# Optimization experiments

Measured on AMD Instinct MI355X. Metric: run time of the kernel, lower is better.

## Reference

```python
import jax, jax.numpy as jnp
import numpy as np

T, B, Y, X, C = 3, 2, 192, 192, 128
H, F = 8, 16
HF = H * F
RY = RX = 2
PH, PW = 2 * RY + 1, 2 * RX + 1
S = PH * PW  # 25 spatial offsets per frame


def setup_inputs() -> dict:
    key = jax.random.key(0)
    ks = jax.random.split(key, 7)
    sc_w = 1.0 / np.sqrt(C)
    return {
        "frames": jax.random.normal(ks[0], (T, B, Y, X, C), jnp.float32),
        "Wq": jax.random.normal(ks[1], (C, HF), jnp.float32) * sc_w,
        "Wk": jax.random.normal(ks[2], (C, HF), jnp.float32) * sc_w,
        "Wv": jax.random.normal(ks[3], (C, HF), jnp.float32) * sc_w,
        "Wout": jax.random.normal(ks[4], (HF, C), jnp.float32) * (1.0 / np.sqrt(HF)),
        "temp_emb": jax.random.normal(ks[5], (T, HF), jnp.float32) * 0.02,
        "spatial_emb": jax.random.normal(ks[6], (S, HF), jnp.float32) * 0.02,
    }


def _attention(frames, Wq, Wk, Wv, Wout, temp_emb, spatial_emb):
    dtype = frames.dtype
    scale = jnp.asarray(1.0 / np.sqrt(F), dtype)
    # 1x1 convs == channel-wise dense
    Kf = jnp.einsum('tbyxc,cd->tbyxd', frames, Wk).reshape(T, B, Y, X, H, F)
    Vf = jnp.einsum('tbyxc,cd->tbyxd', frames, Wv).reshape(T, B, Y, X, H, F)
    Qf = jnp.einsum('tbyxc,cd->tbyxd', frames, Wq).reshape(T, B, Y, X, H, F)
    # temporal embedding: added to K per frame, and to Q per query frame (queries = all frames)
    t_emb = temp_emb.reshape(T, 1, 1, 1, H, F)
    Kf = Kf + t_emb
    # query spatial embedding: relative position of query inside its clipped patch
    yc = jnp.clip(jnp.arange(Y), RY, Y - RY - 1)  # patch center rows [Y]
    xc = jnp.clip(jnp.arange(X), RX, X - RX - 1)  # patch center cols [X]
    y_rel = jnp.arange(Y) - yc + RY
    x_rel = jnp.arange(X) - xc + RX
    q_sidx = y_rel[:, None] * PW + x_rel[None, :]  # [Y,X] in [0,S)
    q_s = spatial_emb[q_sidx].reshape(1, 1, Y, X, H, F)
    Qf = Qf + q_s + t_emb
    # spatial offsets, row-major (dy outer, dx inner) so offset index s matches spatial_emb row
    offs = np.array([[dy, dx] for dy in range(-RY, RY + 1) for dx in range(-RX, RX + 1)], np.int32)
    y_gather = yc[None, :] + jnp.asarray(offs[:, 0])[:, None]  # [S,Y], always in-bounds
    x_gather = xc[None, :] + jnp.asarray(offs[:, 1])[:, None]  # [S,X]
    k_s_emb = spatial_emb.reshape(S, H, F)

    def step(carry, s_in):
        m, l, acc = carry
        yg, xg, ks = s_in  # yg:[Y] xg:[X] ks:[H,F]
        Kg = Kf[:, :, yg][:, :, :, xg] + ks       # [T,B,Y,X,H,F]
        Vg = Vf[:, :, yg][:, :, :, xg]            # [T,B,Y,X,H,F]
        sc = jnp.einsum('qbyxhf,tbyxhf->qtbyxh', Qf, Kg) * scale  # [nQ,T,B,Y,X,H]
        m_new = jnp.maximum(m, sc.max(axis=1))    # [nQ,B,Y,X,H]
        p = jnp.exp(sc - m_new[:, None])
        alpha = jnp.exp(m - m_new)
        l = l * alpha + p.sum(axis=1)
        acc = acc * alpha[..., None] + jnp.einsum('qtbyxh,tbyxhf->qbyxhf', p, Vg)
        return (m_new, l, acc), None

    m0 = jnp.full((T, B, Y, X, H), -1e9, dtype)
    l0 = jnp.zeros((T, B, Y, X, H), dtype)
    acc0 = jnp.zeros((T, B, Y, X, H, F), dtype)
    (m, l, acc), _ = jax.lax.scan(step, (m0, l0, acc0), (y_gather, x_gather, k_s_emb))
    out = (acc / l[..., None]).reshape(T, B, Y, X, HF)
    return jnp.einsum('tbyxd,dc->tbyxc', out, Wout)  # [nQ=T,B,Y,X,C]


def reference(frames, Wq, Wk, Wv, Wout, temp_emb, spatial_emb):
    return _attention(frames, Wq, Wk, Wv, Wout, temp_emb, spatial_emb)
```

## Files before the change

### kernel.cpp

```cpp
#include <hip/hip_runtime.h>
#include <cstdint>
#include <cstddef>

#define T_ 3
#define B_ 2
#define Y_ 192
#define X_ 192
#define YX_ 36864
#define N_ 221184
#define NS_ 73728

typedef __attribute__((ext_vector_type(8))) short short8;
typedef __attribute__((ext_vector_type(4))) float f32x4;
typedef __attribute__((ext_vector_type(2))) float f32x2;
typedef unsigned short u16;
typedef unsigned int u32;

__device__ __forceinline__ u16 f2bf(float f){
  u32 x = __builtin_bit_cast(u32, f);
  x += 0x7fffu + ((x >> 16) & 1u);
  return (u16)(x >> 16);
}
__device__ __forceinline__ float bflo(u32 u){ return __builtin_bit_cast(float, u << 16); }
__device__ __forceinline__ float bfhi(u32 u){ return __builtin_bit_cast(float, u & 0xffff0000u); }
__device__ __forceinline__ f32x2 bfp(u32 u){
  f32x2 r; r.x = bflo(u); r.y = bfhi(u); return r;
}
__device__ __forceinline__ int clampi(int v, int lo, int hi){ return v < lo ? lo : (v > hi ? hi : v); }
__device__ __forceinline__ f32x2 shfl2(f32x2 v, int m){
  f32x2 r; r.x = __shfl_xor(v.x, m); r.y = __shfl_xor(v.y, m); return r;
}

#if __has_builtin(__builtin_amdgcn_fdot2_f32_bf16)
typedef __attribute__((ext_vector_type(2))) __bf16 bf16x2;
__device__ __forceinline__ float dot2bf(u32 a, u32 b, float c){
  return __builtin_amdgcn_fdot2_f32_bf16(__builtin_bit_cast(bf16x2, a),
                                         __builtin_bit_cast(bf16x2, b), c, false);
}
#else
__device__ __forceinline__ float dot2bf(u32 a, u32 b, float c){
  return fmaf(bfhi(a), bfhi(b), fmaf(bflo(a), bflo(b), c));
}
#endif

#if __has_builtin(__builtin_amdgcn_exp2f)
__device__ __forceinline__ float fexp2(float x){ return __builtin_amdgcn_exp2f(x); }
#else
__device__ __forceinline__ float fexp2(float x){ return exp2f(x); }
#endif

#define QSCALE 0.36067376022224085f

__global__ __launch_bounds__(256) void wt_kernel(
    const float* __restrict__ Wq, const float* __restrict__ Wk,
    const float* __restrict__ Wv, const float* __restrict__ Wo,
    const float* __restrict__ spatial_emb, u16* __restrict__ WT, u16* __restrict__ se_bf){
  int idx = blockIdx.x * 256 + threadIdx.x;
  if (idx < 65536){
    int g = idx >> 14;
    int r = (idx >> 7) & 127;
    int c = idx & 127;
    const float* W = (g == 0) ? Wq : (g == 1) ? Wk : (g == 2) ? Wv : Wo;
    WT[g * 16384 + c * 128 + r] = f2bf(W[r * 128 + c]);
  } else if (idx < 65536 + 3200){
    se_bf[idx - 65536] = f2bf(spatial_emb[idx - 65536]);
  }
}

__global__ __launch_bounds__(256, 2) void qkv_kernel(
    const float* __restrict__ frames, const u16* __restrict__ WT,
    u16* __restrict__ Qb, u16* __restrict__ Kb, u16* __restrict__ Vb,
    const float* __restrict__ temp_emb, const float* __restrict__ spatial_emb){
  __shared__ float tile[128 * 128];
  const int tid = threadIdx.x;
  const int w = tid >> 6, l = tid & 63;
  const int l16 = l & 15, lg = l >> 4;
  const int m0 = blockIdx.x * 128;

  short8 af[4][2];
  #pragma unroll
  for (int ks = 0; ks < 4; ++ks)
    #pragma unroll
    for (int mr = 0; mr < 2; ++mr){
      const float* ap = frames + (size_t)(m0 + w * 32 + mr * 16 + l16) * 128 + ks * 32 + lg * 8;
      const f32x4 a0 = *(const f32x4*)ap;
      const f32x4 a1 = *(const f32x4*)(ap + 4);
      short8 t;
      t[0] = (short)f2bf(a0[0]); t[1] = (short)f2bf(a0[1]);
      t[2] = (short)f2bf(a0[2]); t[3] = (short)f2bf(a0[3]);
      t[4] = (short)f2bf(a1[0]); t[5] = (short)f2bf(a1[1]);
      t[6] = (short)f2bf(a1[2]); t[7] = (short)f2bf(a1[3]);
      af[ks][mr] = t;
    }

  #pragma unroll
  for (int g = 0; g < 3; ++g){
    const u16* wt = WT + g * 16384;
    f32x4 acc[2][8];
    #pragma unroll
    for (int mr = 0; mr < 2; ++mr)
      #pragma unroll
      for (int nf = 0; nf < 8; ++nf)
        acc[mr][nf] = (f32x4){0.f, 0.f, 0.f, 0.f};

    #pragma unroll
    for (int ks = 0; ks < 4; ++ks)
      #pragma unroll
      for (int nf = 0; nf < 8; ++nf){
        const short8 bf = *(const short8*)(wt + (nf * 16 + l16) * 128 + ks * 32 + lg * 8);
        acc[0][nf] = __builtin_amdgcn_mfma_f32_16x16x32_bf16(af[ks][0], bf, acc[0][nf], 0, 0, 0);
        acc[1][nf] = __builtin_amdgcn_mfma_f32_16x16x32_bf16(af[ks][1], bf, acc[1][nf], 0, 0, 0);
      }

    if (g > 0) __syncthreads();
    #pragma unroll
    for (int mr = 0; mr < 2; ++mr)
      #pragma unroll
      for (int nf = 0; nf < 8; ++nf)
        #pragma unroll
        for (int i = 0; i < 4; ++i)
          tile[(w * 32 + mr * 16 + lg * 4 + i) * 128 + nf * 16 + l16] = acc[mr][nf][i];
    __syncthreads();

    u16* outp = (g == 0) ? Qb : (g == 1) ? Kb : Vb;
    #pragma unroll
    for (int it = 0; it < 16; ++it){
      const int idx = it * 256 + tid;
      const int r = idx >> 5;
      const int c4 = (idx & 31) * 4;
      f32x4 v = *(const f32x4*)&tile[r * 128 + c4];
      const int p = m0 + r;
      const int t = p / (B_ * YX_);
      if (g <= 1){
        const float* te = temp_emb + t * 128 + c4;
        v[0] += te[0]; v[1] += te[1]; v[2] += te[2]; v[3] += te[3];
      }
      if (g == 0){
        const int yx = p % YX_;
        const int y = yx / X_, x = yx % X_;
        const int yrel = y - clampi(y, 2, Y_ - 3) + 2;
        const int xrel = x - clampi(x, 2, X_ - 3) + 2;
        const float* se = spatial_emb + (yrel * 5 + xrel) * 128 + c4;
        v[0] = (v[0] + se[0]) * QSCALE; v[1] = (v[1] + se[1]) * QSCALE;
        v[2] = (v[2] + se[2]) * QSCALE; v[3] = (v[3] + se[3]) * QSCALE;
      }
      uint2 pk;
      pk.x = (u32)f2bf(v[0]) | ((u32)f2bf(v[1]) << 16);
      pk.y = (u32)f2bf(v[2]) | ((u32)f2bf(v[3]) << 16);
      *(uint2*)(outp + (size_t)p * 128 + c4) = pk;
    }
  }
}

__global__ __attribute__((amdgpu_waves_per_eu(4, 4))) __launch_bounds__(256) void attn_kernel(
    const u16* __restrict__ Kb, const u16* __restrict__ Vb,
    u16* __restrict__ Qb, const u16* __restrict__ se_bf){
  __shared__ float qse[4][2][600];
  __shared__ u32 tbl[80];
  const int tid = threadIdx.x;
  const int w = tid >> 6, l = tid & 63;
  const int s2 = l >> 5, slot = (l >> 3) & 3, h = l & 7;

  if (tid < 80){
    const int kk = tid > 74 ? 74 : tid;
    const int t = kk / 25, s = kk - t * 25;
    const int dy = s / 5, dx = s - dy * 5;
    tbl[tid] = (u32)((((t * (B_ * Y_) + dy) * X_ + dx) * 256) | (s * 8));
  }

  const int site = blockIdx.x * 8 + w * 2 + s2;
  const int b = site / YX_;
  const int yx = site % YX_;
  const int y = yx / X_, x = yx % X_;
  const int yc = clampi(y, 2, 189), xc = clampi(x, 2, 189);
  const u32 sbase = (u32)(((b * Y_ + (yc - 2)) * X_ + (xc - 2)) * 256 + h * 32);
  const char* Kc = (const char*)Kb;
  const char* Vc = (const char*)Vb;

  u32 qp[3][8];
  #pragma unroll
  for (int q = 0; q < 3; ++q){
    const u16* qptr = Qb + ((size_t)((q * B_ + b) * Y_ + y) * X_ + x) * 128 + h * 16;
    const uint4 a = *(const uint4*)qptr;
    const uint4 c = *(const uint4*)(qptr + 8);
    qp[q][0] = a.x; qp[q][1] = a.y; qp[q][2] = a.z; qp[q][3] = a.w;
    qp[q][4] = c.x; qp[q][5] = c.y; qp[q][6] = c.z; qp[q][7] = c.w;
  }

  float* qsl = &qse[w][s2][0];
  #pragma unroll
  for (int sj = 0; sj < 7; ++sj){
    const int so = sj * 4 + slot;
    if (so < 25){
      const u16* sp = se_bf + so * 128 + h * 16;
      const uint4 e0 = *(const uint4*)sp;
      const uint4 e1 = *(const uint4*)(sp + 8);
      u32 ep[8] = {e0.x, e0.y, e0.z, e0.w, e1.x, e1.y, e1.z, e1.w};
      #pragma unroll
      for (int q = 0; q < 3; ++q){
        float d = 0.f;
        #pragma unroll
        for (int i = 0; i < 8; ++i) d = dot2bf(qp[q][i], ep[i], d);
        qsl[q * 200 + so * 8 + h] = d;
      }
    }
  }
  __syncthreads();

  float ll[3] = {0.f, 0.f, 0.f};
  f32x2 acc[3][8];
  #pragma unroll
  for (int q = 0; q < 3; ++q)
    #pragma unroll
    for (int i = 0; i < 8; ++i) acc[q][i] = (f32x2){0.f, 0.f};

  #pragma unroll
  for (int j = 0; j < 19; ++j){
    const int kk = j * 4 + slot;
    const u32 e = tbl[kk];
    const u32 boff = sbase + (e & 0xffffff00u);
    const int s8 = (int)(e & 0xffu);
    const uint4 k0 = *(const uint4*)(Kc + boff);
    const uint4 k1 = *(const uint4*)(Kc + boff + 16);
    const uint4 v0 = *(const uint4*)(Vc + boff);
    const uint4 v1 = *(const uint4*)(Vc + boff + 16);
    const u32 kp[8] = {k0.x, k0.y, k0.z, k0.w, k1.x, k1.y, k1.z, k1.w};
    f32x2 vf[8];
    vf[0] = bfp(v0.x); vf[1] = bfp(v0.y); vf[2] = bfp(v0.z); vf[3] = bfp(v0.w);
    vf[4] = bfp(v1.x); vf[5] = bfp(v1.y); vf[6] = bfp(v1.z); vf[7] = bfp(v1.w);

    #pragma unroll
    for (int q = 0; q < 3; ++q){
      float d = qsl[q * 200 + s8 + h];
      #pragma unroll
      for (int i = 0; i < 8; ++i) d = dot2bf(qp[q][i], kp[i], d);
      float p = fexp2(d);
      if (j == 18 && slot >= 3) p = 0.f;
      ll[q] += p;
      const f32x2 pp = {p, p};
      #pragma unroll
      for (int i = 0; i < 8; ++i) acc[q][i] += pp * vf[i];
    }
  }

  #pragma unroll
  for (int q = 0; q < 3; ++q){
    ll[q] += __shfl_xor(ll[q], 8);
    ll[q] += __shfl_xor(ll[q], 16);
    #pragma unroll
    for (int i = 0; i < 8; ++i){
      acc[q][i] += shfl2(acc[q][i], 8);
      acc[q][i] += shfl2(acc[q][i], 16);
    }
  }

  #pragma unroll
  for (int q = 0; q < 3; ++q){
    if (slot == q){
      const float inv = 1.0f / ll[q];
      uint4 o0, o1;
      {
        const f32x2 t0 = acc[q][0] * inv, t1 = acc[q][1] * inv;
        const f32x2 t2 = acc[q][2] * inv, t3 = acc[q][3] * inv;
        o0.x = (u32)f2bf(t0.x) | ((u32)f2bf(t0.y) << 16);
        o0.y = (u32)f2bf(t1.x) | ((u32)f2bf(t1.y) << 16);
        o0.z = (u32)f2bf(t2.x) | ((u32)f2bf(t2.y) << 16);
        o0.w = (u32)f2bf(t3.x) | ((u32)f2bf(t3.y) << 16);
      }
      {
        const f32x2 t0 = acc[q][4] * inv, t1 = acc[q][5] * inv;
        const f32x2 t2 = acc[q][6] * inv, t3 = acc[q][7] * inv;
        o1.x = (u32)f2bf(t0.x) | ((u32)f2bf(t0.y) << 16);
        o1.y = (u32)f2bf(t1.x) | ((u32)f2bf(t1.y) << 16);
        o1.z = (u32)f2bf(t2.x) | ((u32)f2bf(t2.y) << 16);
        o1.w = (u32)f2bf(t3.x) | ((u32)f2bf(t3.y) << 16);
      }
      u16* dst = Qb + ((size_t)((q * B_ + b) * Y_ + y) * X_ + x) * 128 + h * 16;
      *(uint4*)dst = o0;
      *(uint4*)(dst + 8) = o1;
    }
  }
}

__global__ __launch_bounds__(256) void out_kernel(
    const u16* __restrict__ Ab, const u16* __restrict__ WT3, float* __restrict__ out){
  const int tid = threadIdx.x;
  const int w = tid >> 6, l = tid & 63;
  const int l16 = l & 15, lg = l >> 4;
  const int m0 = blockIdx.x * 128;

  f32x4 acc[2][8];
  #pragma unroll
  for (int mr = 0; mr < 2; ++mr)
    #pragma unroll
    for (int nf = 0; nf < 8; ++nf)
      acc[mr][nf] = (f32x4){0.f, 0.f, 0.f, 0.f};

  #pragma unroll
  for (int ks = 0; ks < 4; ++ks){
    short8 af[2];
    #pragma unroll
    for (int mr = 0; mr < 2; ++mr)
      af[mr] = *(const short8*)(Ab + (size_t)(m0 + w * 32 + mr * 16 + l16) * 128 + ks * 32 + lg * 8);
    #pragma unroll
    for (int nf = 0; nf < 8; ++nf){
      const short8 bf = *(const short8*)(WT3 + (nf * 16 + l16) * 128 + ks * 32 + lg * 8);
      acc[0][nf] = __builtin_amdgcn_mfma_f32_16x16x32_bf16(af[0], bf, acc[0][nf], 0, 0, 0);
      acc[1][nf] = __builtin_amdgcn_mfma_f32_16x16x32_bf16(af[1], bf, acc[1][nf], 0, 0, 0);
    }
  }

  #pragma unroll
  for (int mr = 0; mr < 2; ++mr)
    #pragma unroll
    for (int nf = 0; nf < 8; ++nf)
      #pragma unroll
      for (int i = 0; i < 4; ++i)
        out[(size_t)(m0 + w * 32 + mr * 16 + lg * 4 + i) * 128 + nf * 16 + l16] = acc[mr][nf][i];
}

extern "C" void kernel_launch(void* const* d_in, const int* in_sizes, int n_in,
                              void* d_out, int out_size, void* d_ws, size_t ws_size,
                              hipStream_t stream){
  const float* frames      = (const float*)d_in[0];
  const float* Wq          = (const float*)d_in[1];
  const float* Wk          = (const float*)d_in[2];
  const float* Wv          = (const float*)d_in[3];
  const float* Wo          = (const float*)d_in[4];
  const float* temp_emb    = (const float*)d_in[5];
  const float* spatial_emb = (const float*)d_in[6];

  u16* WT    = (u16*)d_ws;
  u16* se_bf = WT + 4 * 16384;
  u16* Qb    = WT + 68736;
  u16* Kb    = (u16*)d_out;
  u16* Vb    = Kb + (size_t)N_ * 128;
  float* out = (float*)d_out;

  wt_kernel<<<269, 256, 0, stream>>>(Wq, Wk, Wv, Wo, spatial_emb, WT, se_bf);
  qkv_kernel<<<N_ / 128, 256, 0, stream>>>(frames, WT, Qb, Kb, Vb, temp_emb, spatial_emb);
  attn_kernel<<<NS_ / 8, 256, 0, stream>>>(Kb, Vb, Qb, se_bf);
  out_kernel<<<N_ / 128, 256, 0, stream>>>(Qb, WT + 3 * 16384, out);
}
```

Measured before the change: 343.2 us.

## Split each head across two lanes in attention kernel, one site per wave

The attention kernel now gives each lane half of a head's 16 features, so a wave covers one site instead of two. Partial dot products are combined with a lane shuffle, the per-lane accumulator and register footprint halve, and the forced waves-per-EU attribute is removed. The grid doubles to 18432 blocks. The aim is higher occupancy with less register pressure, at the cost of extra shuffles and of doing the exp and softmax bookkeeping twice per head.

New measurement: 411.0 us. 19.7% more time.

```diff
diff --git a/kernel.cpp b/kernel.cpp
--- a/kernel.cpp
+++ b/kernel.cpp
@@ -152,14 +152,15 @@
   }
 }
 
-__global__ __attribute__((amdgpu_waves_per_eu(4, 4))) __launch_bounds__(256) void attn_kernel(
+__global__ __launch_bounds__(256) void attn_kernel(
     const u16* __restrict__ Kb, const u16* __restrict__ Vb,
     u16* __restrict__ Qb, const u16* __restrict__ se_bf){
-  __shared__ float qse[4][2][600];
+  __shared__ float qse[4][600];
   __shared__ u32 tbl[80];
   const int tid = threadIdx.x;
   const int w = tid >> 6, l = tid & 63;
-  const int s2 = l >> 5, slot = (l >> 3) & 3, h = l & 7;
+  const int slot = l >> 4, hh = l & 15;
+  const int h = hh >> 1;
 
   if (tid < 80){
     const int kk = tid > 74 ? 74 : tid;
@@ -168,51 +169,49 @@
     tbl[tid] = (u32)((((t * (B_ * Y_) + dy) * X_ + dx) * 256) | (s * 8));
   }
 
-  const int site = blockIdx.x * 8 + w * 2 + s2;
+  const int site = blockIdx.x * 4 + w;
   const int b = site / YX_;
   const int yx = site % YX_;
   const int y = yx / X_, x = yx % X_;
   const int yc = clampi(y, 2, 189), xc = clampi(x, 2, 189);
-  const u32 sbase = (u32)(((b * Y_ + (yc - 2)) * X_ + (xc - 2)) * 256 + h * 32);
+  const u32 sbase = (u32)(((b * Y_ + (yc - 2)) * X_ + (xc - 2)) * 256 + hh * 16);
   const char* Kc = (const char*)Kb;
   const char* Vc = (const char*)Vb;
 
-  u32 qp[3][8];
+  u32 qp[3][4];
   #pragma unroll
   for (int q = 0; q < 3; ++q){
-    const u16* qptr = Qb + ((size_t)((q * B_ + b) * Y_ + y) * X_ + x) * 128 + h * 16;
+    const u16* qptr = Qb + ((size_t)((q * B_ + b) * Y_ + y) * X_ + x) * 128 + hh * 8;
     const uint4 a = *(const uint4*)qptr;
-    const uint4 c = *(const uint4*)(qptr + 8);
     qp[q][0] = a.x; qp[q][1] = a.y; qp[q][2] = a.z; qp[q][3] = a.w;
-    qp[q][4] = c.x; qp[q][5] = c.y; qp[q][6] = c.z; qp[q][7] = c.w;
-  }
-
-  float* qsl = &qse[w][s2][0];
+  }
+
+  float* qsl = &qse[w][0];
   #pragma unroll
   for (int sj = 0; sj < 7; ++sj){
     const int so = sj * 4 + slot;
     if (so < 25){
-      const u16* sp = se_bf + so * 128 + h * 16;
+      const u16* sp = se_bf + so * 128 + hh * 8;
       const uint4 e0 = *(const uint4*)sp;
-      const uint4 e1 = *(const uint4*)(sp + 8);
-      u32 ep[8] = {e0.x, e0.y, e0.z, e0.w, e1.x, e1.y, e1.z, e1.w};
       #pragma unroll
       for (int q = 0; q < 3; ++q){
-        float d = 0.f;
-        #pragma unroll
-        for (int i = 0; i < 8; ++i) d = dot2bf(qp[q][i], ep[i], d);
-        qsl[q * 200 + so * 8 + h] = d;
+        float d = dot2bf(qp[q][0], e0.x, 0.f);
+        d = dot2bf(qp[q][1], e0.y, d);
+        d = dot2bf(qp[q][2], e0.z, d);
+        d = dot2bf(qp[q][3], e0.w, d);
+        d += __shfl_xor(d, 1);
+        if (!(l & 1)) qsl[q * 200 + so * 8 + h] = d;
       }
     }
   }
   __syncthreads();
 
   float ll[3] = {0.f, 0.f, 0.f};
-  f32x2 acc[3][8];
+  f32x2 acc[3][4];
   #pragma unroll
   for (int q = 0; q < 3; ++q)
     #pragma unroll
-    for (int i = 0; i < 8; ++i) acc[q][i] = (f32x2){0.f, 0.f};
+    for (int i = 0; i < 4; ++i) acc[q][i] = (f32x2){0.f, 0.f};
 
   #pragma unroll
   for (int j = 0; j < 19; ++j){
@@ -220,37 +219,38 @@
     const u32 e = tbl[kk];
     const u32 boff = sbase + (e & 0xffffff00u);
     const int s8 = (int)(e & 0xffu);
-    const uint4 k0 = *(const uint4*)(Kc + boff);
-    const uint4 k1 = *(const uint4*)(Kc + boff + 16);
-    const uint4 v0 = *(const uint4*)(Vc + boff);
-    const uint4 v1 = *(const uint4*)(Vc + boff + 16);
-    const u32 kp[8] = {k0.x, k0.y, k0.z, k0.w, k1.x, k1.y, k1.z, k1.w};
-    f32x2 vf[8];
-    vf[0] = bfp(v0.x); vf[1] = bfp(v0.y); vf[2] = bfp(v0.z); vf[3] = bfp(v0.w);
-    vf[4] = bfp(v1.x); vf[5] = bfp(v1.y); vf[6] = bfp(v1.z); vf[7] = bfp(v1.w);
+    const uint4 ku = *(const uint4*)(Kc + boff);
+    const uint4 vu = *(const uint4*)(Vc + boff);
+    f32x2 vf[4];
+    vf[0] = bfp(vu.x); vf[1] = bfp(vu.y); vf[2] = bfp(vu.z); vf[3] = bfp(vu.w);
 
     #pragma unroll
     for (int q = 0; q < 3; ++q){
-      float d = qsl[q * 200 + s8 + h];
-      #pragma unroll
-      for (int i = 0; i < 8; ++i) d = dot2bf(qp[q][i], kp[i], d);
+      float d = dot2bf(qp[q][0], ku.x, 0.f);
+      d = dot2bf(qp[q][1], ku.y, d);
+      d = dot2bf(qp[q][2], ku.z, d);
+      d = dot2bf(qp[q][3], ku.w, d);
+      d += __shfl_xor(d, 1);
+      d += qsl[q * 200 + s8 + h];
       float p = fexp2(d);
-      if (j == 18 && slot >= 3) p = 0.f;
+      if (j == 18 && slot == 3) p = 0.f;
       ll[q] += p;
       const f32x2 pp = {p, p};
-      #pragma unroll
-      for (int i = 0; i < 8; ++i) acc[q][i] += pp * vf[i];
+      acc[q][0] += pp * vf[0];
+      acc[q][1] += pp * vf[1];
+      acc[q][2] += pp * vf[2];
+      acc[q][3] += pp * vf[3];
     }
   }
 
   #pragma unroll
   for (int q = 0; q < 3; ++q){
-    ll[q] += __shfl_xor(ll[q], 8);
     ll[q] += __shfl_xor(ll[q], 16);
-    #pragma unroll
-    for (int i = 0; i < 8; ++i){
-      acc[q][i] += shfl2(acc[q][i], 8);
+    ll[q] += __shfl_xor(ll[q], 32);
+    #pragma unroll
+    for (int i = 0; i < 4; ++i){
       acc[q][i] += shfl2(acc[q][i], 16);
+      acc[q][i] += shfl2(acc[q][i], 32);
     }
   }
 
@@ -258,26 +258,15 @@
   for (int q = 0; q < 3; ++q){
     if (slot == q){
       const float inv = 1.0f / ll[q];
-      uint4 o0, o1;
-      {
-        const f32x2 t0 = acc[q][0] * inv, t1 = acc[q][1] * inv;
-        const f32x2 t2 = acc[q][2] * inv, t3 = acc[q][3] * inv;
-        o0.x = (u32)f2bf(t0.x) | ((u32)f2bf(t0.y) << 16);
-        o0.y = (u32)f2bf(t1.x) | ((u32)f2bf(t1.y) << 16);
-        o0.z = (u32)f2bf(t2.x) | ((u32)f2bf(t2.y) << 16);
-        o0.w = (u32)f2bf(t3.x) | ((u32)f2bf(t3.y) << 16);
-      }
-      {
-        const f32x2 t0 = acc[q][4] * inv, t1 = acc[q][5] * inv;
-        const f32x2 t2 = acc[q][6] * inv, t3 = acc[q][7] * inv;
-        o1.x = (u32)f2bf(t0.x) | ((u32)f2bf(t0.y) << 16);
-        o1.y = (u32)f2bf(t1.x) | ((u32)f2bf(t1.y) << 16);
-        o1.z = (u32)f2bf(t2.x) | ((u32)f2bf(t2.y) << 16);
-        o1.w = (u32)f2bf(t3.x) | ((u32)f2bf(t3.y) << 16);
-      }
-      u16* dst = Qb + ((size_t)((q * B_ + b) * Y_ + y) * X_ + x) * 128 + h * 16;
-      *(uint4*)dst = o0;
-      *(uint4*)(dst + 8) = o1;
+      const f32x2 t0 = acc[q][0] * inv, t1 = acc[q][1] * inv;
+      const f32x2 t2 = acc[q][2] * inv, t3 = acc[q][3] * inv;
+      uint4 o;
+      o.x = (u32)f2bf(t0.x) | ((u32)f2bf(t0.y) << 16);
+      o.y = (u32)f2bf(t1.x) | ((u32)f2bf(t1.y) << 16);
+      o.z = (u32)f2bf(t2.x) | ((u32)f2bf(t2.y) << 16);
+      o.w = (u32)f2bf(t3.x) | ((u32)f2bf(t3.y) << 16);
+      u16* dst = Qb + ((size_t)((q * B_ + b) * Y_ + y) * X_ + x) * 128 + hh * 8;
+      *(uint4*)dst = o;
     }
   }
 }
@@ -339,6 +328,6 @@
 
   wt_kernel<<<269, 256, 0, stream>>>(Wq, Wk, Wv, Wo, spatial_emb, WT, se_bf);
   qkv_kernel<<<N_ / 128, 256, 0, stream>>>(frames, WT, Qb, Kb, Vb, temp_emb, spatial_emb);
-  attn_kernel<<<NS_ / 8, 256, 0, stream>>>(Kb, Vb, Qb, se_bf);
+  attn_kernel<<<NS_ / 4, 256, 0, stream>>>(Kb, Vb, Qb, se_bf);
   out_kernel<<<N_ / 128, 256, 0, stream>>>(Qb, WT + 3 * 16384, out);
 }
```
